# Kernel tuning notes

Hardware: AMD Instinct MI355X
Metric: run time of the kernel (lower is better)

The kernel has to match this reference:

```python
import jax, jax.numpy as jnp
import numpy as np

N, E, T = 10000, 160000, 1600000
D, C, H = 256, 64, 1024  # d_model, d_message/channels, 4*d_model ffn hidden


def setup_inputs() -> dict:
    key = jax.random.key(0)
    ks = jax.random.split(key, 20)
    rn = lambda k, s, sc=1.0: jax.random.normal(k, s, dtype=jnp.float32) * sc
    return {
        "x": rn(ks[0], (N, D)),
        "y": rn(ks[1], (E, D)),
        "r": rn(ks[2], (E, 3)),
        "src": jax.random.randint(ks[3], (E,), 0, N),
        "dst": jax.random.randint(ks[4], (E,), 0, N),
        "tsrc": jax.random.randint(ks[5], (T,), 0, E),
        "tdst": jax.random.randint(ks[6], (T,), 0, E),
        "W_src": rn(ks[7], (D, C), 0.05), "b_src": rn(ks[8], (C,), 0.05),
        "W_dst": rn(ks[9], (D, C), 0.05), "b_dst": rn(ks[10], (C,), 0.05),
        "W_edge": rn(ks[11], (D, C), 0.05), "b_edge": rn(ks[12], (C,), 0.05),
        "attn": rn(ks[13], (C,), 0.05),
        "W1": rn(ks[14], (C, H), 0.05), "b1": rn(ks[15], (H,), 0.05),
        "W2": rn(ks[16], (H, D), 0.05), "b2": rn(ks[17], (D,), 0.05),
    }


def reference(x, y, r, src, dst, tsrc, tdst,
              W_src, b_src, W_dst, b_dst, W_edge, b_edge,
              attn, W1, b1, W2, b2):
    # per-bond message: xij = Lin_src(x)[src] + Lin_dst(x)[dst] + Lin_edge(y)  -> (E, C)
    xij = (x @ W_src + b_src)[src] + (x @ W_dst + b_dst)[dst] + (y @ W_edge + b_edge)

    # triplet angle cosine via normalized (negated) bond vectors  -> (T,)
    rnorm = -r / jnp.linalg.norm(r, axis=1, keepdims=True)
    cos_jik = jnp.clip(jnp.sum(rnorm[tsrc] * rnorm[tdst], axis=-1), -1.0 + 1e-6, 1.0 - 1e-6)

    # Chebyshev expansion: T_n(cos) = cos(n * arccos(cos))  -> (T, C)
    n = jnp.arange(C, dtype=jnp.float32)
    z_jik = jnp.cos(n[None, :] * jnp.arccos(cos_jik)[:, None])

    # triplet feature and attention logit
    e_jik = jax.nn.silu(z_jik + xij[tsrc] + xij[tdst])          # (T, C)
    logits = e_jik @ attn                                        # (T,)

    # segment softmax over triplets grouped by destination bond (edge_softmax)
    mx = jax.ops.segment_max(logits, tdst, num_segments=E)
    ex = jnp.exp(logits - mx[tdst])
    den = jax.ops.segment_sum(ex, tdst, num_segments=E)
    a = ex / den[tdst]                                           # (T,)

    # attention-weighted scatter-sum of neighbor bond features  -> (E, C)
    ft = jax.ops.segment_sum(xij[tsrc] * a[:, None], tdst, num_segments=E)

    # feedforward: Linear -> SiLU -> Linear  -> (E, D)
    return jax.nn.silu(ft @ W1 + b1) @ W2 + b2
```

## Files before the change

kernel.cpp:

```cpp
#include <hip/hip_runtime.h>

#define N_NODES 10000
#define N_EDGES 160000
#define N_TRI   1600000
#define DM      256
#define CH      64
#define HH      1024

typedef short bf16x8 __attribute__((ext_vector_type(8)));
typedef float f32x4  __attribute__((ext_vector_type(4)));

__device__ __forceinline__ unsigned short f2bf(float f) {
  unsigned int u = __float_as_uint(f);
  u += 0x7fff + ((u >> 16) & 1);
  return (unsigned short)(u >> 16);
}

__global__ __launch_bounds__(256) void k_node_proj(
    const float* __restrict__ x, const float* __restrict__ Ws, const float* __restrict__ bs,
    const float* __restrict__ Wd, const float* __restrict__ bd,
    float* __restrict__ xs, float* __restrict__ xd) {
  __shared__ float xl[4][DM];
  int tid = threadIdx.x;
  int n0 = blockIdx.x * 4;
  for (int i = tid; i < 4 * DM; i += 256) xl[i >> 8][i & 255] = x[n0 * DM + i];
  __syncthreads();
  int c = tid & 63, g = tid >> 6;
  float as = bs[c], ad = bd[c];
  for (int d = 0; d < DM; d++) {
    float xv = xl[g][d];
    as += xv * Ws[d * CH + c];
    ad += xv * Wd[d * CH + c];
  }
  int n = n0 + g;
  xs[n * CH + c] = as;
  xd[n * CH + c] = ad;
}

__global__ __launch_bounds__(256) void k_edge_proj(
    const float* __restrict__ y, const float* __restrict__ We, const float* __restrict__ be,
    const float* __restrict__ xs, const float* __restrict__ xd,
    const int* __restrict__ src, const int* __restrict__ dst,
    float* __restrict__ xij) {
  __shared__ float yl[16][DM];
  int tid = threadIdx.x;
  int e0 = blockIdx.x * 16;
  for (int i = tid; i < 16 * DM; i += 256) yl[i >> 8][i & 255] = y[e0 * DM + i];
  __syncthreads();
  int c = tid & 63, g = tid >> 6;
  float acc[4];
#pragma unroll
  for (int s = 0; s < 4; s++) acc[s] = be[c];
  for (int d = 0; d < DM; d += 4) {
    float w0 = We[(d + 0) * CH + c];
    float w1 = We[(d + 1) * CH + c];
    float w2 = We[(d + 2) * CH + c];
    float w3 = We[(d + 3) * CH + c];
#pragma unroll
    for (int s = 0; s < 4; s++) {
      const float4 yv = *(const float4*)&yl[g * 4 + s][d];
      acc[s] += yv.x * w0 + yv.y * w1 + yv.z * w2 + yv.w * w3;
    }
  }
#pragma unroll
  for (int s = 0; s < 4; s++) {
    int e = e0 + g * 4 + s;
    xij[e * CH + c] = acc[s] + xs[src[e] * CH + c] + xd[dst[e] * CH + c];
  }
}

__global__ void k_rnorm(const float* __restrict__ r, float4* __restrict__ rn4) {
  int e = blockIdx.x * 256 + threadIdx.x;
  if (e >= N_EDGES) return;
  float a = r[e * 3 + 0], b = r[e * 3 + 1], c = r[e * 3 + 2];
  float inv = rsqrtf(a * a + b * b + c * c);
  rn4[e] = (float4){-a * inv, -b * inv, -c * inv, 0.f};
}

__global__ __launch_bounds__(256) void k_theta(
    const float4* __restrict__ rn4, const int* __restrict__ tsrc, const int* __restrict__ tdst,
    float* __restrict__ theta) {
  int t = blockIdx.x * 256 + threadIdx.x;
  if (t >= N_TRI) return;
  float4 a = rn4[tsrc[t]];
  float4 b = rn4[tdst[t]];
  float c = a.x * b.x + a.y * b.y + a.z * b.z;
  c = fminf(fmaxf(c, -1.0f + 1e-6f), 1.0f - 1e-6f);
  theta[t] = acosf(c);
}

__global__ void k_hist(const int* __restrict__ tdst, int* __restrict__ cnt) {
  int t = blockIdx.x * 256 + threadIdx.x;
  if (t < N_TRI) atomicAdd(&cnt[tdst[t]], 1);
}

__global__ __launch_bounds__(256) void k_scan_sum(const int* __restrict__ cnt,
                                                  int* __restrict__ bsum, int n) {
  __shared__ int s[256];
  int b = blockIdx.x, tid = threadIdx.x;
  int tot = 0;
#pragma unroll
  for (int i = 0; i < 8; i++) {
    int idx = b * 2048 + i * 256 + tid;
    if (idx < n) tot += cnt[idx];
  }
  s[tid] = tot;
  __syncthreads();
  for (int off = 128; off > 0; off >>= 1) {
    if (tid < off) s[tid] += s[tid + off];
    __syncthreads();
  }
  if (tid == 0) bsum[b] = s[0];
}

__global__ void k_scan_top(int* __restrict__ bsum, int nb, int* __restrict__ start_last) {
  if (threadIdx.x == 0) {
    int run = 0;
    for (int i = 0; i < nb; i++) {
      int v = bsum[i];
      bsum[i] = run;
      run += v;
    }
    *start_last = run;
  }
}

__global__ __launch_bounds__(256) void k_scan_apply(const int* __restrict__ cnt,
                                                    const int* __restrict__ bsum,
                                                    int* __restrict__ start,
                                                    int* __restrict__ cur, int n) {
  __shared__ int s[256];
  int b = blockIdx.x, tid = threadIdx.x;
  int base = b * 2048 + tid * 8;
  int loc[8];
  int tot = 0;
#pragma unroll
  for (int i = 0; i < 8; i++) {
    int idx = base + i;
    int v = (idx < n) ? cnt[idx] : 0;
    loc[i] = tot;
    tot += v;
  }
  s[tid] = tot;
  __syncthreads();
  for (int off = 1; off < 256; off <<= 1) {
    int t2 = 0;
    if (tid >= off) t2 = s[tid - off];
    __syncthreads();
    if (tid >= off) s[tid] += t2;
    __syncthreads();
  }
  int excl = s[tid] - tot + bsum[b];
#pragma unroll
  for (int i = 0; i < 8; i++) {
    int idx = base + i;
    if (idx < n) {
      int v = excl + loc[i];
      start[idx] = v;
      cur[idx] = v;
    }
  }
}

__global__ void k_scatter(const int* __restrict__ tdst, int* __restrict__ cur,
                          int* __restrict__ sorted) {
  int t = blockIdx.x * 256 + threadIdx.x;
  if (t < N_TRI) {
    int p = atomicAdd(&cur[tdst[t]], 1);
    sorted[p] = t;
  }
}

__global__ __launch_bounds__(256) void k_attn_ft(
    const int* __restrict__ start, const int* __restrict__ sorted,
    const float* __restrict__ theta, const int* __restrict__ tsrc,
    const float* __restrict__ xij, const float* __restrict__ attn,
    unsigned short* __restrict__ ft) {
  int tid = threadIdx.x;
  int e = blockIdx.x * 4 + (tid >> 6);
  int lane = tid & 63;
  float lanef = (float)lane;
  int beg = start[e], end = start[e + 1];
  int deg = end - beg;
  float xd = xij[e * CH + lane];
  float av = attn[lane];
  float m = -1e30f, den = 0.f, acc = 0.f;
  if (deg > 0 && deg <= 64) {
    int ts_ = 0;
    float th_ = 0.f;
    if (lane < deg) {
      int t = sorted[beg + lane];
      ts_ = tsrc[t];
      th_ = theta[t];
    }
    int ts_cur = __shfl(ts_, 0);
    float th_cur = __shfl(th_, 0);
    float xs_cur = xij[ts_cur * CH + lane];
    for (int i = 0; i < deg; i++) {
      float th_nxt = 0.f, xs_nxt = 0.f;
      if (i + 1 < deg) {
        int ts_nxt = __shfl(ts_, i + 1);
        th_nxt = __shfl(th_, i + 1);
        xs_nxt = xij[ts_nxt * CH + lane];
      }
      float v = __cosf(th_cur * lanef) + xs_cur + xd;
      float sv = v / (1.f + __expf(-v));
      float contrib = sv * av;
#pragma unroll
      for (int off = 32; off; off >>= 1) contrib += __shfl_xor(contrib, off);
      float mn = fmaxf(m, contrib);
      float scale = __expf(m - mn);
      float p = __expf(contrib - mn);
      den = den * scale + p;
      acc = acc * scale + p * xs_cur;
      m = mn;
      th_cur = th_nxt;
      xs_cur = xs_nxt;
    }
  } else if (deg > 64) {
    for (int i = 0; i < deg; i++) {
      int t = sorted[beg + i];
      int ts = tsrc[t];
      float th = theta[t];
      float xs = xij[ts * CH + lane];
      float v = __cosf(th * lanef) + xs + xd;
      float sv = v / (1.f + __expf(-v));
      float contrib = sv * av;
#pragma unroll
      for (int off = 32; off; off >>= 1) contrib += __shfl_xor(contrib, off);
      float mn = fmaxf(m, contrib);
      float scale = __expf(m - mn);
      float p = __expf(contrib - mn);
      den = den * scale + p;
      acc = acc * scale + p * xs;
      m = mn;
    }
  }
  ft[e * CH + lane] = f2bf(deg > 0 ? acc / den : 0.f);
}

__global__ __launch_bounds__(256) void k_prep_w1t(const float* __restrict__ W1,
                                                  unsigned short* __restrict__ W1T) {
  int idx = blockIdx.x * 256 + threadIdx.x;
  int n = idx >> 6, k = idx & 63;
  W1T[idx] = f2bf(W1[k * HH + n]);
}

__global__ __launch_bounds__(256) void k_prep_w2t(const float* __restrict__ W2,
                                                  unsigned short* __restrict__ W2T) {
  int idx = blockIdx.x * 256 + threadIdx.x;
  int n = idx >> 10, k = idx & 1023;
  W2T[idx] = f2bf(W2[k * DM + n]);
}

#define HL_STRIDE 72
__global__ __launch_bounds__(256) void k_ffn_mfma(
    const unsigned short* __restrict__ ft, const unsigned short* __restrict__ W1T,
    const float* __restrict__ b1, const unsigned short* __restrict__ W2T,
    const float* __restrict__ b2, float* __restrict__ out) {
  __shared__ unsigned short ftl[64 * 64];
  __shared__ unsigned short hl[2][64 * HL_STRIDE];
  int tid = threadIdx.x;
  int wave = tid >> 6, lane = tid & 63;
  int l16 = lane & 15, lq = lane >> 4;
  int e0 = blockIdx.x * 64;

  {
    const uint* g = (const uint*)(ft + (size_t)e0 * CH);
    uint* s = (uint*)ftl;
    for (int i = tid; i < 64 * 32; i += 256) s[i] = g[i];
  }
  __syncthreads();

  bf16x8 aft[4][2];
#pragma unroll
  for (int mt = 0; mt < 4; mt++)
#pragma unroll
    for (int s = 0; s < 2; s++)
      aft[mt][s] = *(const bf16x8*)&ftl[(mt * 16 + l16) * 64 + s * 32 + lq * 8];

  f32x4 acc[4][4];
#pragma unroll
  for (int mt = 0; mt < 4; mt++)
#pragma unroll
    for (int nt = 0; nt < 4; nt++) acc[mt][nt] = (f32x4){0.f, 0.f, 0.f, 0.f};

  for (int cc = 0; cc < 16; cc++) {
    int p = cc & 1;
    {
      int ncol = cc * 64 + wave * 16 + l16;
      const unsigned short* wp = &W1T[ncol * 64 + lq * 8];
      bf16x8 bw0 = *(const bf16x8*)wp;
      bf16x8 bw1 = *(const bf16x8*)(wp + 32);
      float b1v = b1[ncol];
#pragma unroll
      for (int mt = 0; mt < 4; mt++) {
        f32x4 h = (f32x4){0.f, 0.f, 0.f, 0.f};
        h = __builtin_amdgcn_mfma_f32_16x16x32_bf16(aft[mt][0], bw0, h, 0, 0, 0);
        h = __builtin_amdgcn_mfma_f32_16x16x32_bf16(aft[mt][1], bw1, h, 0, 0, 0);
#pragma unroll
        for (int r = 0; r < 4; r++) {
          float v = h[r] + b1v;
          float sv = v / (1.f + __expf(-v));
          hl[p][(mt * 16 + lq * 4 + r) * HL_STRIDE + wave * 16 + l16] = f2bf(sv);
        }
      }
    }
    __syncthreads();
    bf16x8 ha[4][2];
#pragma unroll
    for (int mt = 0; mt < 4; mt++) {
      ha[mt][0] = *(const bf16x8*)&hl[p][(mt * 16 + l16) * HL_STRIDE + lq * 8];
      ha[mt][1] = *(const bf16x8*)&hl[p][(mt * 16 + l16) * HL_STRIDE + 32 + lq * 8];
    }
#pragma unroll
    for (int nt = 0; nt < 4; nt++) {
      const unsigned short* wp =
          &W2T[(size_t)(wave * 64 + nt * 16 + l16) * HH + cc * 64 + lq * 8];
      bf16x8 b0 = *(const bf16x8*)wp;
      bf16x8 b1f = *(const bf16x8*)(wp + 32);
#pragma unroll
      for (int mt = 0; mt < 4; mt++) {
        acc[mt][nt] = __builtin_amdgcn_mfma_f32_16x16x32_bf16(ha[mt][0], b0, acc[mt][nt], 0, 0, 0);
        acc[mt][nt] = __builtin_amdgcn_mfma_f32_16x16x32_bf16(ha[mt][1], b1f, acc[mt][nt], 0, 0, 0);
      }
    }
  }

#pragma unroll
  for (int nt = 0; nt < 4; nt++) {
    int col = wave * 64 + nt * 16 + l16;
    float b2v = b2[col];
#pragma unroll
    for (int mt = 0; mt < 4; mt++) {
      int row = e0 + mt * 16 + lq * 4;
#pragma unroll
      for (int r = 0; r < 4; r++)
        out[(size_t)(row + r) * DM + col] = acc[mt][nt][r] + b2v;
    }
  }
}

extern "C" void kernel_launch(void* const* d_in, const int* in_sizes, int n_in,
                              void* d_out, int out_size, void* d_ws, size_t ws_size,
                              hipStream_t stream) {
  (void)in_sizes; (void)n_in; (void)out_size; (void)ws_size;
  const float* x      = (const float*)d_in[0];
  const float* y      = (const float*)d_in[1];
  const float* r      = (const float*)d_in[2];
  const int*   src    = (const int*)d_in[3];
  const int*   dst    = (const int*)d_in[4];
  const int*   tsrc   = (const int*)d_in[5];
  const int*   tdst   = (const int*)d_in[6];
  const float* W_src  = (const float*)d_in[7];
  const float* b_src  = (const float*)d_in[8];
  const float* W_dst  = (const float*)d_in[9];
  const float* b_dst  = (const float*)d_in[10];
  const float* W_edge = (const float*)d_in[11];
  const float* b_edge = (const float*)d_in[12];
  const float* attn   = (const float*)d_in[13];
  const float* W1     = (const float*)d_in[14];
  const float* b1     = (const float*)d_in[15];
  const float* W2     = (const float*)d_in[16];
  const float* b2     = (const float*)d_in[17];
  float* out = (float*)d_out;

  char* wsp = (char*)d_ws;
  auto alloc = [&](size_t bytes) -> char* {
    char* p = wsp;
    wsp += (bytes + 255) & ~(size_t)255;
    return p;
  };
  float* xs     = (float*)alloc((size_t)N_NODES * CH * 4);
  float* xd     = (float*)alloc((size_t)N_NODES * CH * 4);
  float* xij    = (float*)alloc((size_t)N_EDGES * CH * 4);
  float4* rn4   = (float4*)alloc((size_t)N_EDGES * 16);
  float* theta  = (float*)alloc((size_t)N_TRI * 4);
  int*   cnt    = (int*)alloc((size_t)N_EDGES * 4);
  int*   start  = (int*)alloc((size_t)(N_EDGES + 1) * 4);
  int*   cur    = (int*)alloc((size_t)N_EDGES * 4);
  int*   bsum   = (int*)alloc(1024 * 4);
  int*   sorted = (int*)alloc((size_t)N_TRI * 4);
  unsigned short* ftb = (unsigned short*)alloc((size_t)N_EDGES * CH * 2);
  unsigned short* W1T = (unsigned short*)alloc((size_t)CH * HH * 2);
  unsigned short* W2T = (unsigned short*)alloc((size_t)HH * DM * 2);

  const int NB = (N_EDGES + 2047) / 2048;

  k_prep_w1t<<<(CH * HH) / 256, 256, 0, stream>>>(W1, W1T);
  k_prep_w2t<<<(HH * DM) / 256, 256, 0, stream>>>(W2, W2T);

  k_node_proj<<<N_NODES / 4, 256, 0, stream>>>(x, W_src, b_src, W_dst, b_dst, xs, xd);
  k_rnorm<<<N_EDGES / 256, 256, 0, stream>>>(r, rn4);
  k_edge_proj<<<N_EDGES / 16, 256, 0, stream>>>(y, W_edge, b_edge, xs, xd, src, dst, xij);
  k_theta<<<N_TRI / 256, 256, 0, stream>>>(rn4, tsrc, tdst, theta);

  hipMemsetAsync(cnt, 0, (size_t)N_EDGES * 4, stream);
  k_hist<<<N_TRI / 256, 256, 0, stream>>>(tdst, cnt);
  k_scan_sum<<<NB, 256, 0, stream>>>(cnt, bsum, N_EDGES);
  k_scan_top<<<1, 64, 0, stream>>>(bsum, NB, &start[N_EDGES]);
  k_scan_apply<<<NB, 256, 0, stream>>>(cnt, bsum, start, cur, N_EDGES);
  k_scatter<<<N_TRI / 256, 256, 0, stream>>>(tdst, cur, sorted);

  k_attn_ft<<<N_EDGES / 4, 256, 0, stream>>>(start, sorted, theta, tsrc, xij, attn, ftb);
  k_ffn_mfma<<<N_EDGES / 64, 256, 0, stream>>>(ftb, W1T, b1, W2T, b2, out);
}
```

Measured before the change: 1.189 ms.

## Keep FFN hidden activations in registers via permuted W1 and transposed MFMA

Reworks the FFN kernel so each wave handles 32 edges and all 256 output columns. It computes the hidden layer as W1·ftᵀ, so the MFMA output layout directly forms the A operand of the second GEMM. W1 is pre-permuted so the accumulator rows land in the needed k order, which removes the shared-memory round-trip and the per-chunk __syncthreads. It also prefetches the next W1 fragment. The cost is a much larger register footprint (128 accumulator floats per lane) and W2 being reloaded per wave rather than shared across the block.

```diff
diff --git a/kernel.cpp b/kernel.cpp
--- a/kernel.cpp
+++ b/kernel.cpp
@@ -239,11 +239,13 @@
   ft[e * CH + lane] = f2bf(deg > 0 ? acc / den : 0.f);
 }
 
-__global__ __launch_bounds__(256) void k_prep_w1t(const float* __restrict__ W1,
-                                                  unsigned short* __restrict__ W1T) {
+__global__ __launch_bounds__(256) void k_prep_w1p(const float* __restrict__ W1,
+                                                  unsigned short* __restrict__ W1P) {
   int idx = blockIdx.x * 256 + threadIdx.x;
-  int n = idx >> 6, k = idx & 63;
-  W1T[idx] = f2bf(W1[k * HH + n]);
+  int k = idx & 63, row = idx >> 6;
+  int i = row & 15, t = (row >> 4) & 1, hb = row >> 5;
+  int hidden = hb * 32 + ((i >> 2) << 3) + (t << 2) + (i & 3);
+  W1P[idx] = f2bf(W1[k * HH + hidden]);
 }
 
 __global__ __launch_bounds__(256) void k_prep_w2t(const float* __restrict__ W2,
@@ -253,90 +255,104 @@
   W2T[idx] = f2bf(W2[k * DM + n]);
 }
 
-#define HL_STRIDE 72
-__global__ __launch_bounds__(256) void k_ffn_mfma(
-    const unsigned short* __restrict__ ft, const unsigned short* __restrict__ W1T,
+__global__ __launch_bounds__(256, 2) void k_ffn_mfma2(
+    const unsigned short* __restrict__ ft, const unsigned short* __restrict__ W1P,
     const float* __restrict__ b1, const unsigned short* __restrict__ W2T,
     const float* __restrict__ b2, float* __restrict__ out) {
-  __shared__ unsigned short ftl[64 * 64];
-  __shared__ unsigned short hl[2][64 * HL_STRIDE];
   int tid = threadIdx.x;
   int wave = tid >> 6, lane = tid & 63;
-  int l16 = lane & 15, lq = lane >> 4;
-  int e0 = blockIdx.x * 64;
-
-  {
-    const uint* g = (const uint*)(ft + (size_t)e0 * CH);
-    uint* s = (uint*)ftl;
-    for (int i = tid; i < 64 * 32; i += 256) s[i] = g[i];
-  }
-  __syncthreads();
-
-  bf16x8 aft[4][2];
-#pragma unroll
-  for (int mt = 0; mt < 4; mt++)
+  int l16 = lane & 15, q = lane >> 4;
+  int ebase = blockIdx.x * 128 + wave * 32;
+
+  bf16x8 ftf[2][2];
+#pragma unroll
+  for (int mt = 0; mt < 2; mt++)
 #pragma unroll
     for (int s = 0; s < 2; s++)
-      aft[mt][s] = *(const bf16x8*)&ftl[(mt * 16 + l16) * 64 + s * 32 + lq * 8];
-
-  f32x4 acc[4][4];
-#pragma unroll
-  for (int mt = 0; mt < 4; mt++)
-#pragma unroll
-    for (int nt = 0; nt < 4; nt++) acc[mt][nt] = (f32x4){0.f, 0.f, 0.f, 0.f};
-
-  for (int cc = 0; cc < 16; cc++) {
-    int p = cc & 1;
-    {
-      int ncol = cc * 64 + wave * 16 + l16;
-      const unsigned short* wp = &W1T[ncol * 64 + lq * 8];
-      bf16x8 bw0 = *(const bf16x8*)wp;
-      bf16x8 bw1 = *(const bf16x8*)(wp + 32);
-      float b1v = b1[ncol];
-#pragma unroll
-      for (int mt = 0; mt < 4; mt++) {
-        f32x4 h = (f32x4){0.f, 0.f, 0.f, 0.f};
-        h = __builtin_amdgcn_mfma_f32_16x16x32_bf16(aft[mt][0], bw0, h, 0, 0, 0);
-        h = __builtin_amdgcn_mfma_f32_16x16x32_bf16(aft[mt][1], bw1, h, 0, 0, 0);
-#pragma unroll
-        for (int r = 0; r < 4; r++) {
-          float v = h[r] + b1v;
-          float sv = v / (1.f + __expf(-v));
-          hl[p][(mt * 16 + lq * 4 + r) * HL_STRIDE + wave * 16 + l16] = f2bf(sv);
-        }
+      ftf[mt][s] = *(const bf16x8*)&ft[(size_t)(ebase + mt * 16 + l16) * CH + s * 32 + q * 8];
+
+  f32x4 acc[2][16];
+#pragma unroll
+  for (int mt = 0; mt < 2; mt++)
+#pragma unroll
+    for (int nt = 0; nt < 16; nt++) acc[mt][nt] = (f32x4){0.f, 0.f, 0.f, 0.f};
+
+  bf16x8 w1f[2][2];
+#pragma unroll
+  for (int t = 0; t < 2; t++)
+#pragma unroll
+    for (int s = 0; s < 2; s++)
+      w1f[t][s] = *(const bf16x8*)&W1P[(size_t)((t * 16) + l16) * 64 + s * 32 + q * 8];
+
+  for (int hb = 0; hb < 32; hb++) {
+    f32x4 h[2][2];
+#pragma unroll
+    for (int mt = 0; mt < 2; mt++)
+#pragma unroll
+      for (int t = 0; t < 2; t++) {
+        f32x4 z = (f32x4){0.f, 0.f, 0.f, 0.f};
+        z = __builtin_amdgcn_mfma_f32_16x16x32_bf16(w1f[t][0], ftf[mt][0], z, 0, 0, 0);
+        z = __builtin_amdgcn_mfma_f32_16x16x32_bf16(w1f[t][1], ftf[mt][1], z, 0, 0, 0);
+        h[mt][t] = z;
       }
-    }
-    __syncthreads();
-    bf16x8 ha[4][2];
-#pragma unroll
-    for (int mt = 0; mt < 4; mt++) {
-      ha[mt][0] = *(const bf16x8*)&hl[p][(mt * 16 + l16) * HL_STRIDE + lq * 8];
-      ha[mt][1] = *(const bf16x8*)&hl[p][(mt * 16 + l16) * HL_STRIDE + 32 + lq * 8];
-    }
-#pragma unroll
-    for (int nt = 0; nt < 4; nt++) {
-      const unsigned short* wp =
-          &W2T[(size_t)(wave * 64 + nt * 16 + l16) * HH + cc * 64 + lq * 8];
-      bf16x8 b0 = *(const bf16x8*)wp;
-      bf16x8 b1f = *(const bf16x8*)(wp + 32);
-#pragma unroll
-      for (int mt = 0; mt < 4; mt++) {
-        acc[mt][nt] = __builtin_amdgcn_mfma_f32_16x16x32_bf16(ha[mt][0], b0, acc[mt][nt], 0, 0, 0);
-        acc[mt][nt] = __builtin_amdgcn_mfma_f32_16x16x32_bf16(ha[mt][1], b1f, acc[mt][nt], 0, 0, 0);
+
+    int hbn = (hb < 31) ? hb + 1 : 31;
+    bf16x8 w1n[2][2];
+#pragma unroll
+    for (int t = 0; t < 2; t++)
+#pragma unroll
+      for (int s = 0; s < 2; s++)
+        w1n[t][s] = *(const bf16x8*)&W1P[(size_t)((hbn * 2 + t) * 16 + l16) * 64 + s * 32 + q * 8];
+
+    const float4 b1v0 = *(const float4*)&b1[hb * 32 + q * 8];
+    const float4 b1v1 = *(const float4*)&b1[hb * 32 + q * 8 + 4];
+    union { bf16x8 v; unsigned int u[4]; } pa[2];
+#pragma unroll
+    for (int mt = 0; mt < 2; mt++) {
+      float v0 = h[mt][0][0] + b1v0.x, v1 = h[mt][0][1] + b1v0.y;
+      float v2 = h[mt][0][2] + b1v0.z, v3 = h[mt][0][3] + b1v0.w;
+      float w0 = h[mt][1][0] + b1v1.x, w1 = h[mt][1][1] + b1v1.y;
+      float w2 = h[mt][1][2] + b1v1.z, w3 = h[mt][1][3] + b1v1.w;
+      float s0 = v0 / (1.f + __expf(-v0)), s1 = v1 / (1.f + __expf(-v1));
+      float s2 = v2 / (1.f + __expf(-v2)), s3 = v3 / (1.f + __expf(-v3));
+      float t0 = w0 / (1.f + __expf(-w0)), t1 = w1 / (1.f + __expf(-w1));
+      float t2 = w2 / (1.f + __expf(-w2)), t3 = w3 / (1.f + __expf(-w3));
+      pa[mt].u[0] = ((unsigned int)f2bf(s1) << 16) | f2bf(s0);
+      pa[mt].u[1] = ((unsigned int)f2bf(s3) << 16) | f2bf(s2);
+      pa[mt].u[2] = ((unsigned int)f2bf(t1) << 16) | f2bf(t0);
+      pa[mt].u[3] = ((unsigned int)f2bf(t3) << 16) | f2bf(t2);
+    }
+
+#pragma unroll
+    for (int ng = 0; ng < 4; ng++) {
+      bf16x8 bw[4];
+#pragma unroll
+      for (int i = 0; i < 4; i++)
+        bw[i] = *(const bf16x8*)&W2T[(size_t)((ng * 4 + i) * 16 + l16) * HH + hb * 32 + q * 8];
+#pragma unroll
+      for (int i = 0; i < 4; i++) {
+        acc[0][ng * 4 + i] =
+            __builtin_amdgcn_mfma_f32_16x16x32_bf16(pa[0].v, bw[i], acc[0][ng * 4 + i], 0, 0, 0);
+        acc[1][ng * 4 + i] =
+            __builtin_amdgcn_mfma_f32_16x16x32_bf16(pa[1].v, bw[i], acc[1][ng * 4 + i], 0, 0, 0);
       }
     }
-  }
-
-#pragma unroll
-  for (int nt = 0; nt < 4; nt++) {
-    int col = wave * 64 + nt * 16 + l16;
-    float b2v = b2[col];
-#pragma unroll
-    for (int mt = 0; mt < 4; mt++) {
-      int row = e0 + mt * 16 + lq * 4;
+
+#pragma unroll
+    for (int t = 0; t < 2; t++)
+#pragma unroll
+      for (int s = 0; s < 2; s++) w1f[t][s] = w1n[t][s];
+  }
+
+#pragma unroll
+  for (int nt = 0; nt < 16; nt++) {
+    float b2v = b2[nt * 16 + l16];
+#pragma unroll
+    for (int mt = 0; mt < 2; mt++) {
+      int erow = ebase + mt * 16 + q * 4;
 #pragma unroll
       for (int r = 0; r < 4; r++)
-        out[(size_t)(row + r) * DM + col] = acc[mt][nt][r] + b2v;
+        out[(size_t)(erow + r) * DM + nt * 16 + l16] = acc[mt][nt][r] + b2v;
     }
   }
 }
@@ -382,12 +398,12 @@
   int*   bsum   = (int*)alloc(1024 * 4);
   int*   sorted = (int*)alloc((size_t)N_TRI * 4);
   unsigned short* ftb = (unsigned short*)alloc((size_t)N_EDGES * CH * 2);
-  unsigned short* W1T = (unsigned short*)alloc((size_t)CH * HH * 2);
+  unsigned short* W1P = (unsigned short*)alloc((size_t)CH * HH * 2);
   unsigned short* W2T = (unsigned short*)alloc((size_t)HH * DM * 2);
 
   const int NB = (N_EDGES + 2047) / 2048;
 
-  k_prep_w1t<<<(CH * HH) / 256, 256, 0, stream>>>(W1, W1T);
+  k_prep_w1p<<<(CH * HH) / 256, 256, 0, stream>>>(W1, W1P);
   k_prep_w2t<<<(HH * DM) / 256, 256, 0, stream>>>(W2, W2T);
 
   k_node_proj<<<N_NODES / 4, 256, 0, stream>>>(x, W_src, b_src, W_dst, b_dst, xs, xd);
@@ -403,5 +419,5 @@
   k_scatter<<<N_TRI / 256, 256, 0, stream>>>(tdst, cur, sorted);
 
   k_attn_ft<<<N_EDGES / 4, 256, 0, stream>>>(start, sorted, theta, tsrc, xij, attn, ftb);
-  k_ffn_mfma<<<N_EDGES / 64, 256, 0, stream>>>(ftb, W1T, b1, W2T, b2, out);
-}
+  k_ffn_mfma2<<<N_EDGES / 128, 256, 0, stream>>>(ftb, W1P, b1, W2T, b2, out);
+}
```

Measured after the change: 1.318 ms. +10.8%, slower.
